# Performance work log

Measured on AMD Instinct MI355X. Metric: run time of the kernel, lower is better.

Reference implementation:

```python
import jax, jax.numpy as jnp
import numpy as np

B, S, H, E, K = 4, 2048, 1024, 8, 2


def setup_inputs() -> dict:
    key = jax.random.key(0)
    k0, k1, k2 = jax.random.split(key, 3)
    x = jax.random.normal(k0, (B, S, H), dtype=jnp.float32)
    # gate: Linear(H -> E); torch stores W as [out,in], we keep [E,H]
    gate_w = jax.random.normal(k1, (E, H), dtype=jnp.float32) * 0.02
    gate_b = jnp.zeros((E,), dtype=jnp.float32)
    # experts: E x Linear(H -> H); stored as [E, H_in, H_out]
    expert_w = jax.random.normal(k2, (E, H, H), dtype=jnp.float32) * 0.02
    expert_b = jnp.zeros((E, H), dtype=jnp.float32)
    return {"x": x, "gate_w": gate_w, "gate_b": gate_b,
            "expert_w": expert_w, "expert_b": expert_b}


def reference(x, gate_w, gate_b, expert_w, expert_b):
    bsz, seq_len, h = x.shape
    xt = x.reshape(-1, h)                      # [T, H]
    T = xt.shape[0]

    # router (moe_router): softmax -> top-k -> renormalize
    logits = xt @ gate_w.T + gate_b            # [T, E]
    routing_probs = jax.nn.softmax(logits, axis=-1)
    top_k_probs, top_k_index = jax.lax.top_k(routing_probs, K)
    top_k_probs = top_k_probs / jnp.sum(top_k_probs, axis=1, keepdims=True)
    top_k_probs = top_k_probs.astype(x.dtype)

    # combine weights: scatter normalized top-k probs into [T, E]
    rows = jnp.arange(T)[:, None]
    combine = jnp.zeros((T, E), dtype=x.dtype).at[rows, top_k_index].add(top_k_probs)

    # per-expert FFN over all tokens, then weighted combine
    # (equivalent math to the gather / index_add loop: zero weights contribute zero)
    y = jnp.einsum('th,eho->teo', xt, expert_w) + expert_b[None, :, :]  # [T, E, H]
    out = jnp.einsum('te,teh->th', combine, y)                          # [T, H]

    final_output = out.reshape(bsz, seq_len, h)
    return final_output, top_k_index, routing_probs
```

## Files before the change

### kernel.cpp

```cpp
#include <hip/hip_runtime.h>
#include <hip/hip_bf16.h>
#include <stdint.h>

typedef unsigned short ushort_t;
typedef __bf16 bf16x8 __attribute__((ext_vector_type(8)));
typedef float f32x4 __attribute__((ext_vector_type(4)));

#define T_TOK 8192
#define H_DIM 1024
#define E_EXP 8
#define BM 256
#define BN 256
#define BK 64
#define NKT (H_DIM / BK)
#define NITER (NKT / 2)
#define NWG_G 512

#define CNT_STRIDE 64
#define RTOK 32
#define RBLOCKS (T_TOK / RTOK)
#define TP_BLOCKS ((H_DIM / 32) * (H_DIM / 32) * E_EXP)

static __device__ __forceinline__ ushort_t f2bf(float f) {
  union { float f; uint32_t u; } c; c.f = f;
  uint32_t u = c.u;
  uint32_t r = u + 0x7FFFu + ((u >> 16) & 1u);
  return (ushort_t)(r >> 16);
}

__global__ __launch_bounds__(256) void router_transpose(
    const float* __restrict__ x, const float* __restrict__ gw,
    const float* __restrict__ gb, const float* __restrict__ ew,
    float* __restrict__ out_idx, float* __restrict__ out_probs,
    int* __restrict__ counts, int* __restrict__ tok, float* __restrict__ wts,
    ushort_t* __restrict__ xg, ushort_t* __restrict__ wT)
{
  __shared__ ushort_t xrow[RTOK][H_DIM];
  __shared__ int   sm_eid[RTOK * 2];
  __shared__ float sm_wt[RTOK * 2];
  __shared__ int   sm_dst[RTOK * 2];
  __shared__ int   lcnt[E_EXP], lbase[E_EXP], lpos[E_EXP];
  __shared__ float tile[32][33];

  const int tid = threadIdx.x;

  if (blockIdx.x >= RBLOCKS) {
    const int tb = blockIdx.x - RBLOCKS;
    const int e = tb >> 10;
    const int n0 = (tb & 31) * 32, k0 = ((tb >> 5) & 31) * 32;
    const float* we = ew + (size_t)e * H_DIM * H_DIM;
    ushort_t* wTe = wT + (size_t)e * H_DIM * H_DIM;
    const int tx = tid & 31, ty = tid >> 5;
#pragma unroll
    for (int i = 0; i < 4; i++)
      tile[ty + 8 * i][tx] = we[(size_t)(k0 + ty + 8 * i) * H_DIM + n0 + tx];
    __syncthreads();
#pragma unroll
    for (int i = 0; i < 4; i++)
      wTe[(size_t)(n0 + ty + 8 * i) * H_DIM + k0 + tx] = f2bf(tile[tx][ty + 8 * i]);
    return;
  }

  const int wave = tid >> 6, l = tid & 63;
  if (tid < E_EXP) { lcnt[tid] = 0; lpos[tid] = 0; }
  __syncthreads();

  const int t0 = blockIdx.x * RTOK;
  for (int it = 0; it < RTOK / 4; it++) {
    const int lt = wave * (RTOK / 4) + it;
    const int t = t0 + lt;
    const float* xt = x + (size_t)t * H_DIM;
    float acc[E_EXP];
#pragma unroll
    for (int e = 0; e < E_EXP; e++) acc[e] = 0.f;
#pragma unroll
    for (int i = 0; i < 4; i++) {
      const int h = (i * 64 + l) * 4;
      const float4 xv = *reinterpret_cast<const float4*>(xt + h);
      ushort4 b;
      b.x = f2bf(xv.x); b.y = f2bf(xv.y); b.z = f2bf(xv.z); b.w = f2bf(xv.w);
      *reinterpret_cast<ushort4*>(&xrow[lt][h]) = b;
#pragma unroll
      for (int e = 0; e < E_EXP; e++) {
        const float4 g = *reinterpret_cast<const float4*>(gw + e * H_DIM + h);
        acc[e] += xv.x * g.x + xv.y * g.y + xv.z * g.z + xv.w * g.w;
      }
    }
#pragma unroll
    for (int e = 0; e < E_EXP; e++) {
      float v = acc[e];
#pragma unroll
      for (int off = 32; off; off >>= 1) v += __shfl_xor(v, off);
      acc[e] = v;
    }
    if (l == 0) {
      float lg[E_EXP], pb[E_EXP];
      float m = -1e30f;
#pragma unroll
      for (int e = 0; e < E_EXP; e++) { lg[e] = acc[e] + gb[e]; m = fmaxf(m, lg[e]); }
      float s = 0.f;
#pragma unroll
      for (int e = 0; e < E_EXP; e++) { pb[e] = expf(lg[e] - m); s += pb[e]; }
      const float inv = 1.f / s;
#pragma unroll
      for (int e = 0; e < E_EXP; e++) {
        pb[e] *= inv;
        out_probs[(size_t)t * E_EXP + e] = pb[e];
      }
      int i0 = 0; float p0 = pb[0];
#pragma unroll
      for (int e = 1; e < E_EXP; e++) if (pb[e] > p0) { p0 = pb[e]; i0 = e; }
      int i1 = -1; float p1 = -1.f;
#pragma unroll
      for (int e = 0; e < E_EXP; e++) if (e != i0 && pb[e] > p1) { p1 = pb[e]; i1 = e; }
      out_idx[(size_t)t * 2 + 0] = (float)i0;
      out_idx[(size_t)t * 2 + 1] = (float)i1;
      const float rn = 1.f / (p0 + p1);
      sm_eid[lt * 2 + 0] = i0; sm_wt[lt * 2 + 0] = p0 * rn;
      sm_eid[lt * 2 + 1] = i1; sm_wt[lt * 2 + 1] = p1 * rn;
    }
  }
  __syncthreads();

  if (tid < RTOK * 2) atomicAdd(&lcnt[sm_eid[tid]], 1);
  __syncthreads();
  if (tid < E_EXP) lbase[tid] = atomicAdd(&counts[tid * CNT_STRIDE], lcnt[tid]);
  __syncthreads();
  if (tid < RTOK * 2) {
    const int e = sm_eid[tid];
    const int p = lbase[e] + atomicAdd(&lpos[e], 1);
    const int dst = e * T_TOK + p;
    tok[dst] = (t0 + (tid >> 1)) * 2 + (tid & 1);
    wts[dst] = sm_wt[tid];
    sm_dst[tid] = dst;
  }
  __syncthreads();

  for (int ent0 = 0; ent0 < RTOK * 2; ent0 += 4) {
    const int ent = ent0 + wave;
    const int dst = sm_dst[ent];
    const ushort_t* src = &xrow[ent >> 1][0];
    ushort_t* d = xg + (size_t)dst * H_DIM;
    const int o = l * 16;
    *reinterpret_cast<int4*>(d + o) = *reinterpret_cast<const int4*>(src + o);
    *reinterpret_cast<int4*>(d + o + 8) =
        *reinterpret_cast<const int4*>(src + o + 8);
  }
}

#define GLDS16(gp, lp)                                                         \
  __builtin_amdgcn_global_load_lds(                                            \
      (const __attribute__((address_space(1))) void*)(gp),                     \
      (__attribute__((address_space(3))) void*)(lp), 16, 0, 0)

#define WAITV6() asm volatile("s_waitcnt vmcnt(6)" ::: "memory")
#define WAITV0() asm volatile("s_waitcnt vmcnt(0)" ::: "memory")
#define LGKM0()                                                                \
  do {                                                                         \
    asm volatile("s_waitcnt lgkmcnt(0)" ::: "memory");                         \
    __builtin_amdgcn_sched_barrier(0);                                         \
  } while (0)
#define BAR()                                                                  \
  do {                                                                         \
    __builtin_amdgcn_sched_barrier(0);                                         \
    __builtin_amdgcn_s_barrier();                                              \
    __builtin_amdgcn_sched_barrier(0);                                         \
  } while (0)

__global__ __launch_bounds__(512, 2) void moe_gemm(
    const ushort_t* __restrict__ xg, const ushort_t* __restrict__ wT,
    const float* __restrict__ bias, int* __restrict__ counts,
    const int* __restrict__ tok, const float* __restrict__ wts,
    ushort_t* __restrict__ y)
{
  __shared__ __align__(16) ushort_t AsR[2 * 2 * BM * 32];
  __shared__ __align__(16) ushort_t BsR[2 * 2 * BM * 32];
  __shared__ int stok[BM];
  __shared__ float swt[BM];
  __shared__ int s_spill;
#define AS_(buf, kh, idx) AsR[((buf) * 2 + (kh)) * 8192 + (idx)]
#define BS_(buf, kh, idx) BsR[((buf) * 2 + (kh)) * 8192 + (idx)]

  const int tid = threadIdx.x;
  const int bid = blockIdx.x;

  int ne[E_EXP], fl[E_EXP];
#pragma unroll
  for (int i = 0; i < E_EXP; i++) {
    ne[i] = counts[i * CNT_STRIDE];
    fl[i] = ne[i] >> 8;
  }

  const int l = tid & 63;
  const int wid = tid >> 6;
  const int fr = l & 15;
  const int g = l >> 4;

  if (bid < 256) {
    int e = bid & 7;
    int q = bid >> 3;
    const int home = fl[e] * 4;
    if (q >= (home < 32 ? home : 32)) {
      int sc[E_EXP], spill_total = 0;
#pragma unroll
      for (int i = 0; i < E_EXP; i++) {
        sc[i] = fl[i] * 4 > 32 ? fl[i] * 4 - 32 : 0;
        spill_total += sc[i];
      }
      if (spill_total == 0) return;
      if (tid == 0) s_spill = atomicAdd(&counts[520], 1);
      __syncthreads();
      int k = s_spill;
      if (k >= spill_total) return;
      int done = 0;
#pragma unroll
      for (int i = 0; i < E_EXP; i++) {
        if (!done) { if (k < sc[i]) { e = i; done = 1; } else k -= sc[i]; }
      }
      q = 32 + k;
    }
    const int mt = q >> 2;
    const int nt = q & 3;

    if (tid < BM) {
      stok[tid] = tok[e * T_TOK + mt * BM + tid];
      swt[tid] = wts[e * T_TOK + mt * BM + tid];
    }
    __syncthreads();

    const int r0 = tid >> 2;
    const int cp = (tid & 3) ^ ((tid >> 3) & 3);
    const ushort_t* wTe = wT + (size_t)e * H_DIM * H_DIM;
    const ushort_t* aBase = xg + (size_t)(e * T_TOK + mt * BM) * H_DIM;
    const ushort_t* aP0 = aBase + (size_t)r0 * H_DIM + cp * 8;
    const ushort_t* aP1 = aBase + (size_t)(r0 + 128) * H_DIM + cp * 8;
    const ushort_t* bP0 = wTe + (size_t)(nt * BN + r0) * H_DIM + cp * 8;
    const ushort_t* bP1 = wTe + (size_t)(nt * BN + r0 + 128) * H_DIM + cp * 8;
    const int d0 = tid * 8;
    const int d1 = (tid + 512) * 8;

#define STAGE_A(t, kh, buf)                                                    \
  do {                                                                         \
    GLDS16(aP0 + (t) * BK + (kh) * 32, &AS_((buf), (kh), d0));                 \
    GLDS16(aP1 + (t) * BK + (kh) * 32, &AS_((buf), (kh), d1));                 \
  } while (0)
#define STAGE_B(t, kh, buf)                                                    \
  do {                                                                         \
    GLDS16(bP0 + (t) * BK + (kh) * 32, &BS_((buf), (kh), d0));                 \
    GLDS16(bP1 + (t) * BK + (kh) * 32, &BS_((buf), (kh), d1));                 \
  } while (0)

    const int wm = wid >> 2, wn = wid & 3;
    const int sl = g ^ ((l >> 1) & 3);
    const int arow0 = wm * 128 + fr;
    const int brow0 = wn * 64 + fr;

    bf16x8 af[8], bv[2];
    f32x4 acc[8][4] = {};

#define READ_A(buf, kk)                                                        \
  do {                                                                         \
    _Pragma("unroll") for (int mi = 0; mi < 8; mi++)                           \
        af[mi] = *reinterpret_cast<const bf16x8*>(                             \
            &AS_((buf), (kk), (arow0 + mi * 16) * 32 + sl * 8));               \
  } while (0)
#define READ_B(buf, kk, nh)                                                    \
  do {                                                                         \
    _Pragma("unroll") for (int j = 0; j < 2; j++)                              \
        bv[j] = *reinterpret_cast<const bf16x8*>(                              \
            &BS_((buf), (kk), (brow0 + ((nh) * 2 + j) * 16) * 32 + sl * 8));   \
  } while (0)
#define MFMA16(nh)                                                             \
  do {                                                                         \
    __builtin_amdgcn_s_setprio(1);                                             \
    _Pragma("unroll") for (int mi = 0; mi < 8; mi++)                           \
        _Pragma("unroll") for (int j = 0; j < 2; j++)                          \
            acc[mi][(nh) * 2 + j] = __builtin_amdgcn_mfma_f32_16x16x32_bf16(   \
                af[mi], bv[j], acc[mi][(nh) * 2 + j], 0, 0, 0);                \
    __builtin_amdgcn_s_setprio(0);                                             \
  } while (0)

#define ITER_BODY(TT, MORE)                                                    \
  do {                                                                         \
                                                                       \
    READ_A(0, 0); READ_B(0, 0, 0);                                             \
    STAGE_B((TT) + 1, 1, 1);                                                   \
    BAR(); LGKM0(); MFMA16(0); BAR();                                          \
                                                                       \
    READ_B(0, 0, 1);                                                           \
    if (MORE) STAGE_A((TT) + 2, 0, 0);                                         \
    BAR(); LGKM0(); MFMA16(1); BAR();                                          \
                                                                       \
    READ_A(0, 1); READ_B(0, 1, 0);                                             \
    if (MORE) STAGE_B((TT) + 2, 0, 0);                                         \
    BAR(); LGKM0(); MFMA16(0); BAR();                                          \
                                               \
    READ_B(0, 1, 1);                                                           \
    if (MORE) { STAGE_A((TT) + 2, 1, 0); WAITV6(); } else { WAITV0(); }        \
    BAR(); LGKM0(); MFMA16(1); BAR();                                          \
                                                                       \
    READ_A(1, 0); READ_B(1, 0, 0);                                             \
    if (MORE) STAGE_B((TT) + 2, 1, 0);                                         \
    BAR(); LGKM0(); MFMA16(0); BAR();                                          \
                                                                       \
    READ_B(1, 0, 1);                                                           \
    if (MORE) STAGE_A((TT) + 3, 0, 1);                                         \
    BAR(); LGKM0(); MFMA16(1); BAR();                                          \
                                                                       \
    READ_A(1, 1); READ_B(1, 1, 0);                                             \
    if (MORE) STAGE_B((TT) + 3, 0, 1);                                         \
    BAR(); LGKM0(); MFMA16(0); BAR();                                          \
                                               \
    READ_B(1, 1, 1);                                                           \
    if (MORE) { STAGE_A((TT) + 3, 1, 1); WAITV6(); }                           \
    BAR(); LGKM0(); MFMA16(1); BAR();                                          \
  } while (0)

    STAGE_A(0, 0, 0); STAGE_B(0, 0, 0); STAGE_A(0, 1, 0); STAGE_B(0, 1, 0);
    STAGE_A(1, 0, 1); STAGE_B(1, 0, 1); STAGE_A(1, 1, 1);
    WAITV6();
    BAR();

#pragma unroll 1
    for (int it = 0; it < NITER - 1; ++it) {
      const int t = 2 * it;
      ITER_BODY(t, 1);
    }
    {
      const int t = 2 * (NITER - 1);
      ITER_BODY(t, 0);
    }

    float bias4[4];
#pragma unroll
    for (int nj = 0; nj < 4; nj++)
      bias4[nj] = bias[e * H_DIM + nt * BN + wn * 64 + nj * 16 + fr];
#pragma unroll
    for (int mi = 0; mi < 8; mi++) {
      const int rr0 = wm * 128 + mi * 16 + g * 4;
#pragma unroll
      for (int r = 0; r < 4; r++) {
        const int row = rr0 + r;
        const float wgt = swt[row];
        ushort_t* yr = y + (size_t)stok[row] * H_DIM;
#pragma unroll
        for (int nj = 0; nj < 4; nj++) {
          const int n = nt * BN + wn * 64 + nj * 16 + fr;
          yr[n] = f2bf(wgt * (acc[mi][nj][r] + bias4[nj]));
        }
      }
    }
  } else {
    const int e = bid & 7;
    const int tq = (bid - 256) >> 3;
    const int rem = ne[e] - (fl[e] << 8);
    const int tcnt = (rem + 63) >> 6;
    if (tq >= tcnt * 8) return;
    const int mtt = tq >> 3;
    const int ntt = tq & 7;
    const int row0 = (fl[e] << 8) + mtt * 64;
    int valid = ne[e] - row0; if (valid > 64) valid = 64;

    if (tid < 64) {
      int slot = row0 + tid;
      if (slot >= ne[e]) slot = ne[e] - 1;
      stok[tid] = tok[e * T_TOK + slot];
      swt[tid] = wts[e * T_TOK + slot];
    }
    __syncthreads();

    const ushort_t* wTe = wT + (size_t)e * H_DIM * H_DIM;
    const int trow = tid >> 3;
    const int tlc = (tid & 7) ^ (trow & 7);
    int tsl = row0 + trow;
    if (tsl >= ne[e]) tsl = ne[e] - 1;
    const ushort_t* taS = xg + (size_t)(e * T_TOK + tsl) * H_DIM + tlc * 8;
    const ushort_t* tbS0 = wTe + (size_t)(ntt * 128 + trow) * H_DIM + tlc * 8;
    const ushort_t* tbS1 = tbS0 + (size_t)64 * H_DIM;

#define TSTAGE(t, buf)                                                         \
  do {                                                                         \
    GLDS16(taS + (t) * BK, &AsR[(buf) * 4096 + tid * 8]);                      \
    GLDS16(tbS0 + (t) * BK, &BsR[(buf) * 8192 + tid * 8]);                     \
    GLDS16(tbS1 + (t) * BK, &BsR[(buf) * 8192 + (tid + 512) * 8]);             \
  } while (0)

    const int tph0 = (g ^ (fr & 7)) * 8;
    const int tph1 = ((4 ^ g) ^ (fr & 7)) * 8;

    f32x4 tacc[4] = {};

    TSTAGE(0, 0);
    WAITV0();
    BAR();

#pragma unroll
    for (int t = 0; t < NKT; ++t) {
      if (t + 1 < NKT) TSTAGE(t + 1, (t + 1) & 1);
      const ushort_t* Ab = &AsR[(t & 1) * 4096];
      const ushort_t* Bb = &BsR[(t & 1) * 8192];
#pragma unroll
      for (int kk = 0; kk < 2; kk++) {
        const int ph = kk ? tph1 : tph0;
        const bf16x8 tbv = *reinterpret_cast<const bf16x8*>(
            &Bb[(wid * 16 + fr) * 64 + ph]);
#pragma unroll
        for (int mi = 0; mi < 4; mi++) {
          const bf16x8 tav = *reinterpret_cast<const bf16x8*>(
              &Ab[(mi * 16 + fr) * 64 + ph]);
          tacc[mi] = __builtin_amdgcn_mfma_f32_16x16x32_bf16(
              tav, tbv, tacc[mi], 0, 0, 0);
        }
      }
      WAITV0();
      BAR();
    }

    const int ncol = ntt * 128 + wid * 16 + fr;
    const float bs = bias[e * H_DIM + ncol];
#pragma unroll
    for (int mi = 0; mi < 4; mi++) {
      const int rb = mi * 16 + g * 4;
#pragma unroll
      for (int r = 0; r < 4; r++) {
        const int row = rb + r;
        if (row < valid) {
          ushort_t* yr = y + (size_t)stok[row] * H_DIM;
          yr[ncol] = f2bf(swt[row] * (tacc[mi][r] + bs));
        }
      }
    }
  }
}

__global__ __launch_bounds__(256) void combine_kernel(
    const ushort_t* __restrict__ y, float* __restrict__ out)
{
  const int t = blockIdx.x;
  const ushort_t* r0 = y + (size_t)(t * 2) * H_DIM;
  const ushort_t* r1 = r0 + H_DIM;
  float* o = out + (size_t)t * H_DIM;
  const int h = threadIdx.x * 4;
  const ushort4 u0 = *reinterpret_cast<const ushort4*>(r0 + h);
  const ushort4 u1 = *reinterpret_cast<const ushort4*>(r1 + h);
  float4 v;
  union { uint32_t u; float f; } c;
  c.u = (uint32_t)u0.x << 16; v.x = c.f; c.u = (uint32_t)u1.x << 16; v.x += c.f;
  c.u = (uint32_t)u0.y << 16; v.y = c.f; c.u = (uint32_t)u1.y << 16; v.y += c.f;
  c.u = (uint32_t)u0.z << 16; v.z = c.f; c.u = (uint32_t)u1.z << 16; v.z += c.f;
  c.u = (uint32_t)u0.w << 16; v.w = c.f; c.u = (uint32_t)u1.w << 16; v.w += c.f;
  *reinterpret_cast<float4*>(o + h) = v;
}

extern "C" void kernel_launch(void* const* d_in, const int* in_sizes, int n_in,
                              void* d_out, int out_size, void* d_ws, size_t ws_size,
                              hipStream_t stream)
{
  const float* x  = (const float*)d_in[0];
  const float* gw = (const float*)d_in[1];
  const float* gb = (const float*)d_in[2];
  const float* ew = (const float*)d_in[3];
  const float* eb = (const float*)d_in[4];

  float* out = (float*)d_out;
  float* out_final = out;
  float* out_idx   = out + (size_t)T_TOK * H_DIM;
  float* out_probs = out_idx + (size_t)T_TOK * 2;

  char* ws = (char*)d_ws;
  size_t off = 0;
  int*      counts  = (int*)(ws + off); off += 4096;
  int*      tok     = (int*)(ws + off); off += (size_t)E_EXP * T_TOK * 4;
  float*    wts     = (float*)(ws + off); off += (size_t)E_EXP * T_TOK * 4;
  ushort_t* wT      = (ushort_t*)(ws + off); off += (size_t)E_EXP * H_DIM * H_DIM * 2;
  ushort_t* y       = (ushort_t*)(ws + off); off += (size_t)T_TOK * 2 * H_DIM * 2;
  ushort_t* xg      = (ushort_t*)(ws + off); off += (size_t)E_EXP * T_TOK * H_DIM * 2;

  hipMemsetAsync(counts, 0, 4096, stream);

  router_transpose<<<RBLOCKS + TP_BLOCKS, 256, 0, stream>>>(
      x, gw, gb, ew, out_idx, out_probs, counts, tok, wts, xg, wT);
  moe_gemm<<<NWG_G, 512, 0, stream>>>(xg, wT, eb, counts, tok, wts, y);
  combine_kernel<<<T_TOK, 256, 0, stream>>>(y, out_final);
}
```

Measured before the change: 97.56 us.

## Shrink MoE GEMM tiles to 128x128 with 256-thread workgroups and more blocks

Cuts the grouped GEMM macro tile from 256x256 to 128x128 and the workgroup from 512 to 256 threads, raising the grid from 512 to 1280 workgroups and remapping the home/spill tile scheduling to match. The tail path is reworked for 256 threads, with each wave now covering two N fragments. The aim is better load balance and CU occupancy given uneven expert token counts. In exchange, operand reuse per tile drops, so more global/LDS traffic is needed per FLOP.

Result: slower. 107.2 us (+9.9%).

```diff
diff --git a/kernel.cpp b/kernel.cpp
--- a/kernel.cpp
+++ b/kernel.cpp
@@ -9,12 +9,12 @@
 #define T_TOK 8192
 #define H_DIM 1024
 #define E_EXP 8
-#define BM 256
-#define BN 256
+#define BM 128
+#define BN 128
 #define BK 64
 #define NKT (H_DIM / BK)
 #define NITER (NKT / 2)
-#define NWG_G 512
+#define NWG_G 1280
 
 #define CNT_STRIDE 64
 #define RTOK 32
@@ -167,7 +167,7 @@
     __builtin_amdgcn_sched_barrier(0);                                         \
   } while (0)
 
-__global__ __launch_bounds__(512, 2) void moe_gemm(
+__global__ __launch_bounds__(256, 2) void moe_gemm(
     const ushort_t* __restrict__ xg, const ushort_t* __restrict__ wT,
     const float* __restrict__ bias, int* __restrict__ counts,
     const int* __restrict__ tok, const float* __restrict__ wts,
@@ -178,8 +178,8 @@
   __shared__ int stok[BM];
   __shared__ float swt[BM];
   __shared__ int s_spill;
-#define AS_(buf, kh, idx) AsR[((buf) * 2 + (kh)) * 8192 + (idx)]
-#define BS_(buf, kh, idx) BsR[((buf) * 2 + (kh)) * 8192 + (idx)]
+#define AS_(buf, kh, idx) AsR[((buf) * 2 + (kh)) * 4096 + (idx)]
+#define BS_(buf, kh, idx) BsR[((buf) * 2 + (kh)) * 4096 + (idx)]
 
   const int tid = threadIdx.x;
   const int bid = blockIdx.x;
@@ -188,7 +188,7 @@
 #pragma unroll
   for (int i = 0; i < E_EXP; i++) {
     ne[i] = counts[i * CNT_STRIDE];
-    fl[i] = ne[i] >> 8;
+    fl[i] = ne[i] >> 7;
   }
 
   const int l = tid & 63;
@@ -196,15 +196,15 @@
   const int fr = l & 15;
   const int g = l >> 4;
 
-  if (bid < 256) {
+  if (bid < 1024) {
     int e = bid & 7;
     int q = bid >> 3;
-    const int home = fl[e] * 4;
-    if (q >= (home < 32 ? home : 32)) {
+    const int home = fl[e] * 8;
+    if (q >= (home < 128 ? home : 128)) {
       int sc[E_EXP], spill_total = 0;
 #pragma unroll
       for (int i = 0; i < E_EXP; i++) {
-        sc[i] = fl[i] * 4 > 32 ? fl[i] * 4 - 32 : 0;
+        sc[i] = fl[i] * 8 > 128 ? fl[i] * 8 - 128 : 0;
         spill_total += sc[i];
       }
       if (spill_total == 0) return;
@@ -217,10 +217,10 @@
       for (int i = 0; i < E_EXP; i++) {
         if (!done) { if (k < sc[i]) { e = i; done = 1; } else k -= sc[i]; }
       }
-      q = 32 + k;
-    }
-    const int mt = q >> 2;
-    const int nt = q & 3;
+      q = 128 + k;
+    }
+    const int mt = q >> 3;
+    const int nt = q & 7;
 
     if (tid < BM) {
       stok[tid] = tok[e * T_TOK + mt * BM + tid];
@@ -233,11 +233,11 @@
     const ushort_t* wTe = wT + (size_t)e * H_DIM * H_DIM;
     const ushort_t* aBase = xg + (size_t)(e * T_TOK + mt * BM) * H_DIM;
     const ushort_t* aP0 = aBase + (size_t)r0 * H_DIM + cp * 8;
-    const ushort_t* aP1 = aBase + (size_t)(r0 + 128) * H_DIM + cp * 8;
+    const ushort_t* aP1 = aBase + (size_t)(r0 + 64) * H_DIM + cp * 8;
     const ushort_t* bP0 = wTe + (size_t)(nt * BN + r0) * H_DIM + cp * 8;
-    const ushort_t* bP1 = wTe + (size_t)(nt * BN + r0 + 128) * H_DIM + cp * 8;
+    const ushort_t* bP1 = wTe + (size_t)(nt * BN + r0 + 64) * H_DIM + cp * 8;
     const int d0 = tid * 8;
-    const int d1 = (tid + 512) * 8;
+    const int d1 = (tid + 256) * 8;
 
 #define STAGE_A(t, kh, buf)                                                    \
   do {                                                                         \
@@ -250,17 +250,17 @@
     GLDS16(bP1 + (t) * BK + (kh) * 32, &BS_((buf), (kh), d1));                 \
   } while (0)
 
-    const int wm = wid >> 2, wn = wid & 3;
+    const int wm = wid >> 1, wn = wid & 1;
     const int sl = g ^ ((l >> 1) & 3);
-    const int arow0 = wm * 128 + fr;
+    const int arow0 = wm * 64 + fr;
     const int brow0 = wn * 64 + fr;
 
-    bf16x8 af[8], bv[2];
-    f32x4 acc[8][4] = {};
+    bf16x8 af[4], bv[2];
+    f32x4 acc[4][4] = {};
 
 #define READ_A(buf, kk)                                                        \
   do {                                                                         \
-    _Pragma("unroll") for (int mi = 0; mi < 8; mi++)                           \
+    _Pragma("unroll") for (int mi = 0; mi < 4; mi++)                           \
         af[mi] = *reinterpret_cast<const bf16x8*>(                             \
             &AS_((buf), (kk), (arow0 + mi * 16) * 32 + sl * 8));               \
   } while (0)
@@ -270,10 +270,10 @@
         bv[j] = *reinterpret_cast<const bf16x8*>(                              \
             &BS_((buf), (kk), (brow0 + ((nh) * 2 + j) * 16) * 32 + sl * 8));   \
   } while (0)
-#define MFMA16(nh)                                                             \
+#define MFMA8(nh)                                                              \
   do {                                                                         \
     __builtin_amdgcn_s_setprio(1);                                             \
-    _Pragma("unroll") for (int mi = 0; mi < 8; mi++)                           \
+    _Pragma("unroll") for (int mi = 0; mi < 4; mi++)                           \
         _Pragma("unroll") for (int j = 0; j < 2; j++)                          \
             acc[mi][(nh) * 2 + j] = __builtin_amdgcn_mfma_f32_16x16x32_bf16(   \
                 af[mi], bv[j], acc[mi][(nh) * 2 + j], 0, 0, 0);                \
@@ -285,35 +285,35 @@
                                                                        \
     READ_A(0, 0); READ_B(0, 0, 0);                                             \
     STAGE_B((TT) + 1, 1, 1);                                                   \
-    BAR(); LGKM0(); MFMA16(0); BAR();                                          \
+    BAR(); LGKM0(); MFMA8(0); BAR();                                           \
                                                                        \
     READ_B(0, 0, 1);                                                           \
     if (MORE) STAGE_A((TT) + 2, 0, 0);                                         \
-    BAR(); LGKM0(); MFMA16(1); BAR();                                          \
+    BAR(); LGKM0(); MFMA8(1); BAR();                                           \
                                                                        \
     READ_A(0, 1); READ_B(0, 1, 0);                                             \
     if (MORE) STAGE_B((TT) + 2, 0, 0);                                         \
-    BAR(); LGKM0(); MFMA16(0); BAR();                                          \
+    BAR(); LGKM0(); MFMA8(0); BAR();                                           \
                                                \
     READ_B(0, 1, 1);                                                           \
     if (MORE) { STAGE_A((TT) + 2, 1, 0); WAITV6(); } else { WAITV0(); }        \
-    BAR(); LGKM0(); MFMA16(1); BAR();                                          \
+    BAR(); LGKM0(); MFMA8(1); BAR();                                           \
                                                                        \
     READ_A(1, 0); READ_B(1, 0, 0);                                             \
     if (MORE) STAGE_B((TT) + 2, 1, 0);                                         \
-    BAR(); LGKM0(); MFMA16(0); BAR();                                          \
+    BAR(); LGKM0(); MFMA8(0); BAR();                                           \
                                                                        \
     READ_B(1, 0, 1);                                                           \
     if (MORE) STAGE_A((TT) + 3, 0, 1);                                         \
-    BAR(); LGKM0(); MFMA16(1); BAR();                                          \
+    BAR(); LGKM0(); MFMA8(1); BAR();                                           \
                                                                        \
     READ_A(1, 1); READ_B(1, 1, 0);                                             \
     if (MORE) STAGE_B((TT) + 3, 0, 1);                                         \
-    BAR(); LGKM0(); MFMA16(0); BAR();                                          \
+    BAR(); LGKM0(); MFMA8(0); BAR();                                           \
                                                \
     READ_B(1, 1, 1);                                                           \
     if (MORE) { STAGE_A((TT) + 3, 1, 1); WAITV6(); }                           \
-    BAR(); LGKM0(); MFMA16(1); BAR();                                          \
+    BAR(); LGKM0(); MFMA8(1); BAR();                                           \
   } while (0)
 
     STAGE_A(0, 0, 0); STAGE_B(0, 0, 0); STAGE_A(0, 1, 0); STAGE_B(0, 1, 0);
@@ -336,8 +336,8 @@
     for (int nj = 0; nj < 4; nj++)
       bias4[nj] = bias[e * H_DIM + nt * BN + wn * 64 + nj * 16 + fr];
 #pragma unroll
-    for (int mi = 0; mi < 8; mi++) {
-      const int rr0 = wm * 128 + mi * 16 + g * 4;
+    for (int mi = 0; mi < 4; mi++) {
+      const int rr0 = wm * 64 + mi * 16 + g * 4;
 #pragma unroll
       for (int r = 0; r < 4; r++) {
         const int row = rr0 + r;
@@ -352,13 +352,13 @@
     }
   } else {
     const int e = bid & 7;
-    const int tq = (bid - 256) >> 3;
-    const int rem = ne[e] - (fl[e] << 8);
+    const int tq = (bid - 1024) >> 3;
+    const int rem = ne[e] - (fl[e] << 7);
     const int tcnt = (rem + 63) >> 6;
     if (tq >= tcnt * 8) return;
     const int mtt = tq >> 3;
     const int ntt = tq & 7;
-    const int row0 = (fl[e] << 8) + mtt * 64;
+    const int row0 = (fl[e] << 7) + mtt * 64;
     int valid = ne[e] - row0; if (valid > 64) valid = 64;
 
     if (tid < 64) {
@@ -372,23 +372,29 @@
     const ushort_t* wTe = wT + (size_t)e * H_DIM * H_DIM;
     const int trow = tid >> 3;
     const int tlc = (tid & 7) ^ (trow & 7);
-    int tsl = row0 + trow;
-    if (tsl >= ne[e]) tsl = ne[e] - 1;
-    const ushort_t* taS = xg + (size_t)(e * T_TOK + tsl) * H_DIM + tlc * 8;
+    int tsl0 = row0 + trow;       if (tsl0 >= ne[e]) tsl0 = ne[e] - 1;
+    int tsl1 = row0 + trow + 32;  if (tsl1 >= ne[e]) tsl1 = ne[e] - 1;
+    const ushort_t* taS0 = xg + (size_t)(e * T_TOK + tsl0) * H_DIM + tlc * 8;
+    const ushort_t* taS1 = xg + (size_t)(e * T_TOK + tsl1) * H_DIM + tlc * 8;
     const ushort_t* tbS0 = wTe + (size_t)(ntt * 128 + trow) * H_DIM + tlc * 8;
-    const ushort_t* tbS1 = tbS0 + (size_t)64 * H_DIM;
+    const ushort_t* tbS1 = tbS0 + (size_t)32 * H_DIM;
+    const ushort_t* tbS2 = tbS0 + (size_t)64 * H_DIM;
+    const ushort_t* tbS3 = tbS0 + (size_t)96 * H_DIM;
 
 #define TSTAGE(t, buf)                                                         \
   do {                                                                         \
-    GLDS16(taS + (t) * BK, &AsR[(buf) * 4096 + tid * 8]);                      \
+    GLDS16(taS0 + (t) * BK, &AsR[(buf) * 4096 + tid * 8]);                     \
+    GLDS16(taS1 + (t) * BK, &AsR[(buf) * 4096 + (tid + 256) * 8]);             \
     GLDS16(tbS0 + (t) * BK, &BsR[(buf) * 8192 + tid * 8]);                     \
-    GLDS16(tbS1 + (t) * BK, &BsR[(buf) * 8192 + (tid + 512) * 8]);             \
+    GLDS16(tbS1 + (t) * BK, &BsR[(buf) * 8192 + (tid + 256) * 8]);             \
+    GLDS16(tbS2 + (t) * BK, &BsR[(buf) * 8192 + (tid + 512) * 8]);             \
+    GLDS16(tbS3 + (t) * BK, &BsR[(buf) * 8192 + (tid + 768) * 8]);             \
   } while (0)
 
     const int tph0 = (g ^ (fr & 7)) * 8;
     const int tph1 = ((4 ^ g) ^ (fr & 7)) * 8;
 
-    f32x4 tacc[4] = {};
+    f32x4 tacc[2][4] = {};
 
     TSTAGE(0, 0);
     WAITV0();
@@ -402,31 +408,37 @@
 #pragma unroll
       for (int kk = 0; kk < 2; kk++) {
         const int ph = kk ? tph1 : tph0;
-        const bf16x8 tbv = *reinterpret_cast<const bf16x8*>(
-            &Bb[(wid * 16 + fr) * 64 + ph]);
-#pragma unroll
-        for (int mi = 0; mi < 4; mi++) {
-          const bf16x8 tav = *reinterpret_cast<const bf16x8*>(
-              &Ab[(mi * 16 + fr) * 64 + ph]);
-          tacc[mi] = __builtin_amdgcn_mfma_f32_16x16x32_bf16(
-              tav, tbv, tacc[mi], 0, 0, 0);
+#pragma unroll
+        for (int nf = 0; nf < 2; nf++) {
+          const bf16x8 tbv = *reinterpret_cast<const bf16x8*>(
+              &Bb[(wid * 32 + nf * 16 + fr) * 64 + ph]);
+#pragma unroll
+          for (int mi = 0; mi < 4; mi++) {
+            const bf16x8 tav = *reinterpret_cast<const bf16x8*>(
+                &Ab[(mi * 16 + fr) * 64 + ph]);
+            tacc[nf][mi] = __builtin_amdgcn_mfma_f32_16x16x32_bf16(
+                tav, tbv, tacc[nf][mi], 0, 0, 0);
+          }
         }
       }
       WAITV0();
       BAR();
     }
 
-    const int ncol = ntt * 128 + wid * 16 + fr;
-    const float bs = bias[e * H_DIM + ncol];
-#pragma unroll
-    for (int mi = 0; mi < 4; mi++) {
-      const int rb = mi * 16 + g * 4;
-#pragma unroll
-      for (int r = 0; r < 4; r++) {
-        const int row = rb + r;
-        if (row < valid) {
-          ushort_t* yr = y + (size_t)stok[row] * H_DIM;
-          yr[ncol] = f2bf(swt[row] * (tacc[mi][r] + bs));
+#pragma unroll
+    for (int nf = 0; nf < 2; nf++) {
+      const int ncol = ntt * 128 + wid * 32 + nf * 16 + fr;
+      const float bs = bias[e * H_DIM + ncol];
+#pragma unroll
+      for (int mi = 0; mi < 4; mi++) {
+        const int rb = mi * 16 + g * 4;
+#pragma unroll
+        for (int r = 0; r < 4; r++) {
+          const int row = rb + r;
+          if (row < valid) {
+            ushort_t* yr = y + (size_t)stok[row] * H_DIM;
+            yr[ncol] = f2bf(swt[row] * (tacc[nf][mi][r] + bs));
+          }
         }
       }
     }
@@ -480,6 +492,6 @@
 
   router_transpose<<<RBLOCKS + TP_BLOCKS, 256, 0, stream>>>(
       x, gw, gb, ew, out_idx, out_probs, counts, tok, wts, xg, wT);
-  moe_gemm<<<NWG_G, 512, 0, stream>>>(xg, wT, eb, counts, tok, wts, y);
+  moe_gemm<<<NWG_G, 256, 0, stream>>>(xg, wT, eb, counts, tok, wts, y);
   combine_kernel<<<T_TOK, 256, 0, stream>>>(y, out_final);
 }
```
